# Kernel tuning notes

Measured on AMD Instinct MI355X. Metric: run time of the kernel, lower is better.

## Reference

```python
import jax, jax.numpy as jnp
import numpy as np

B, S, H = 2, 2048, 2048
E, K, HID = 8, 2, 4096          # num_experts, top-k, expert hidden (2*H)
NH, HD = 8, 256                  # attention heads, head_dim
MS, MD = 256, 512                # memory_size, memory_dim
RSTEPS, RD = 3, 512              # reasoning steps, reasoning_dim
SCALE = 16.0                     # sqrt(head_dim)


def setup_inputs() -> dict:
    key = jax.random.key(0)
    ks = iter(jax.random.split(key, 64))
    def w(shape, s=0.02):
        return (jax.random.normal(next(ks), shape, jnp.float32) * s)
    z = lambda *shape: jnp.zeros(shape, jnp.float32)
    inp = {
        'hidden_states': jax.random.normal(next(ks), (B, S, H), jnp.float32),
        'attention_mask': jnp.zeros((B, S), jnp.float32),  # 0 = unmasked (faithful: mask*-1e9 added)
        # MoE
        'gate_w': w((H, E)), 'gate_b': z(E),
        'moe_w1': w((E, H, HID)), 'moe_b1': z(E, HID),
        'moe_w2': w((E, HID, H)), 'moe_b2': z(E, H),
        # memory-augmented attention
        'q_w': w((H, H)), 'q_b': z(H),
        'k_w': w((H, H)), 'k_b': z(H),
        'v_w': w((H, H)), 'v_b': z(H),
        'o_w': w((H, H)), 'o_b': z(H),
        'mem_values': jax.random.normal(next(ks), (MS, MD), jnp.float32),
        'mem_proj_w': w((MD, H)), 'mem_proj_b': z(H),
        'mem_attn_w': w((H, MS)), 'mem_attn_b': z(MS),
        # hierarchical reasoning (stacked over steps)
        'rs_w1': w((RSTEPS, H, RD)), 'rs_b1': z(RSTEPS, RD),
        'rs_w2': w((RSTEPS, RD, H)), 'rs_b2': z(RSTEPS, H),
        'ln_g': jnp.ones((RSTEPS, H), jnp.float32), 'ln_b': z(RSTEPS, H),
        'hg_w1': w((RSTEPS, H, H // 4)), 'hg_b1': z(RSTEPS, H // 4),
        'hg_w2': w((RSTEPS, H // 4, 1)), 'hg_b2': z(RSTEPS, 1),
        'integ_w': w((RSTEPS * H, H)), 'integ_b': z(H),
    }
    return inp


def _layernorm(x, g, b, eps=1e-5):
    m = x.mean(-1, keepdims=True)
    v = ((x - m) ** 2).mean(-1, keepdims=True)
    return (x - m) / jnp.sqrt(v + eps) * g + b


def _forward(hidden_states, attention_mask, gate_w, gate_b, moe_w1, moe_b1, moe_w2, moe_b2,
             q_w, q_b, k_w, k_b, v_w, v_b, o_w, o_b, mem_values, mem_proj_w, mem_proj_b,
             mem_attn_w, mem_attn_b, rs_w1, rs_b1, rs_w2, rs_b2, ln_g, ln_b,
             hg_w1, hg_b1, hg_w2, hg_b2, integ_w, integ_b):
    h = hidden_states
    N = B * S
    # ---- Mixture of Experts (top-k routing, dense combine-weight formulation) ----
    x_flat = h.reshape(N, H)
    gate_probs = jax.nn.softmax(x_flat @ gate_w + gate_b, axis=-1)        # [N,E]
    topk_s, topk_i = jax.lax.top_k(gate_probs, K)                          # [N,K]
    topk_p = jax.nn.softmax(topk_s, axis=-1)                               # renormalize over top-k
    comb = jnp.zeros((N, E), x_flat.dtype).at[jnp.arange(N)[:, None], topk_i].add(topk_p)
    h1 = jax.nn.relu(jnp.einsum('nd,edh->neh', x_flat, moe_w1) + moe_b1)   # [N,E,HID]
    eo = jnp.einsum('neh,ehd->ned', h1, moe_w2) + moe_b2                   # [N,E,H]
    moe_out = jnp.einsum('ned,ne->nd', eo, comb).reshape(B, S, H)
    h = h + 0.5 * moe_out
    # ---- Memory-augmented attention ----
    q = (h @ q_w + q_b).reshape(B, S, NH, HD).transpose(0, 2, 1, 3)
    k = (h @ k_w + k_b).reshape(B, S, NH, HD).transpose(0, 2, 1, 3)
    v = (h @ v_w + v_b).reshape(B, S, NH, HD).transpose(0, 2, 1, 3)
    scores = jnp.einsum('bhqd,bhkd->bhqk', q, k) / SCALE
    scores = scores + attention_mask[:, None, None, :] * (-1e9)
    probs = jax.nn.softmax(scores, axis=-1)
    attn = jnp.einsum('bhqk,bhkd->bhqd', probs, v).transpose(0, 2, 1, 3).reshape(B, S, H)
    mem_p = jax.nn.softmax(h @ mem_attn_w + mem_attn_b, axis=-1)           # [B,S,MS]
    mem_o = (mem_p @ mem_values) @ mem_proj_w + mem_proj_b                 # [B,S,H]
    mem_out = (attn + 0.3 * mem_o) @ o_w + o_b
    h = h + mem_out
    # ---- Hierarchical reasoning ----
    cur = h
    outs = []
    for i in range(RSTEPS):
        so = jax.nn.relu(cur @ rs_w1[i] + rs_b1[i]) @ rs_w2[i] + rs_b2[i]
        so = _layernorm(so, ln_g[i], ln_b[i])
        g = jax.nn.sigmoid(jax.nn.relu(cur @ hg_w1[i] + hg_b1[i]) @ hg_w2[i] + hg_b2[i])  # [B,S,1]
        cur = cur + g * so
        outs.append(cur)
    final = jnp.concatenate(outs, axis=-1) @ integ_w + integ_b
    return h + final


def reference(hidden_states, attention_mask, gate_w, gate_b, moe_w1, moe_b1, moe_w2, moe_b2,
              q_w, q_b, k_w, k_b, v_w, v_b, o_w, o_b, mem_values, mem_proj_w, mem_proj_b,
              mem_attn_w, mem_attn_b, rs_w1, rs_b1, rs_w2, rs_b2, ln_g, ln_b,
              hg_w1, hg_b1, hg_w2, hg_b2, integ_w, integ_b):
    return _forward(hidden_states, attention_mask, gate_w, gate_b, moe_w1, moe_b1, moe_w2, moe_b2,
                    q_w, q_b, k_w, k_b, v_w, v_b, o_w, o_b, mem_values, mem_proj_w, mem_proj_b,
                    mem_attn_w, mem_attn_b, rs_w1, rs_b1, rs_w2, rs_b2, ln_g, ln_b,
                    hg_w1, hg_b1, hg_w2, hg_b2, integ_w, integ_b)
```

## Files before the change

### kernel.cpp

```cpp
#include <hip/hip_runtime.h>
#include <string.h>


typedef __attribute__((ext_vector_type(4))) float f32x4;
typedef __attribute__((ext_vector_type(8))) __bf16 bf16x8;

#define NTOK 4096
#define HDIM 2048

__device__ __forceinline__ unsigned short f2bf(float f) {
  unsigned u = __float_as_uint(f);
  unsigned r = (u + 0x7fffu + ((u >> 16) & 1u)) >> 16;
  return (unsigned short)r;
}
__device__ __forceinline__ float bf2f(unsigned short u) {
  return __uint_as_float(((unsigned)u) << 16);
}
__device__ __forceinline__ void unpack8(uint4 r, float* v) {
  v[0]=bf2f((unsigned short)(r.x&0xffff)); v[1]=bf2f((unsigned short)(r.x>>16));
  v[2]=bf2f((unsigned short)(r.y&0xffff)); v[3]=bf2f((unsigned short)(r.y>>16));
  v[4]=bf2f((unsigned short)(r.z&0xffff)); v[5]=bf2f((unsigned short)(r.z>>16));
  v[6]=bf2f((unsigned short)(r.w&0xffff)); v[7]=bf2f((unsigned short)(r.w>>16));
}
__device__ __forceinline__ uint4 pack8(const float* v) {
  uint4 r;
  r.x = (unsigned)f2bf(v[0]) | ((unsigned)f2bf(v[1])<<16);
  r.y = (unsigned)f2bf(v[2]) | ((unsigned)f2bf(v[3])<<16);
  r.z = (unsigned)f2bf(v[4]) | ((unsigned)f2bf(v[5])<<16);
  r.w = (unsigned)f2bf(v[6]) | ((unsigned)f2bf(v[7])<<16);
  return r;
}

__global__ void k_tconv(const float* __restrict__ in, unsigned short* __restrict__ out,
                        int R, int C, long inB, long outB) {
  __shared__ float tl[32][33];
  const int z = blockIdx.z;
  const float* ip = in + (long)z * inB;
  unsigned short* op = out + (long)z * outB;
  const int tx = threadIdx.x & 31, ty = threadIdx.x >> 5;
  const int c0 = blockIdx.x * 32, r0 = blockIdx.y * 32;
#pragma unroll
  for (int i = 0; i < 4; i++)
    tl[ty + i*8][tx] = ip[(long)(r0 + ty + i*8) * C + c0 + tx];
  __syncthreads();
#pragma unroll
  for (int i = 0; i < 4; i++)
    op[(long)(c0 + ty + i*8) * R + r0 + tx] = f2bf(tl[tx][ty + i*8]);
}

__global__ void k_cvt(const float* __restrict__ in, unsigned short* __restrict__ out, long n4) {
  long i = (long)blockIdx.x * blockDim.x + threadIdx.x;
  if (i < n4) {
    float4 v = ((const float4*)in)[i];
    float vv[4] = {v.x, v.y, v.z, v.w};
    union { unsigned short u[4]; uint2 d; } p;
#pragma unroll
    for (int j = 0; j < 4; j++) p.u[j] = f2bf(vv[j]);
    ((uint2*)out)[i] = p.d;
  }
}

__global__ void k_tvact(const unsigned short* __restrict__ qkv, unsigned short* __restrict__ vT) {
  __shared__ unsigned short tl[32][33];
  const int z = blockIdx.z, b = z >> 3, hh = z & 7;
  const unsigned short* ip = qkv + (long)b * 2048 * 6144 + 4096 + hh * 256;
  unsigned short* op = vT + (long)z * 256 * 2048;
  const int tx = threadIdx.x & 31, ty = threadIdx.x >> 5;
  const int d0 = blockIdx.x * 32, s0 = blockIdx.y * 32;
#pragma unroll
  for (int i = 0; i < 4; i++)
    tl[ty + i*8][tx] = ip[(long)(s0 + ty + i*8) * 6144 + d0 + tx];
  __syncthreads();
#pragma unroll
  for (int i = 0; i < 4; i++)
    op[(long)(d0 + ty + i*8) * 2048 + s0 + tx] = tl[tx][ty + i*8];
}

__global__ void k_maskvec(const float* __restrict__ m, float* __restrict__ mv) {
  int i = blockIdx.x * 256 + threadIdx.x;
  if (i < 4096) mv[i] = -1e9f * m[i];
}

__global__ void k_zero(int* p) { if (threadIdx.x < 8) p[threadIdx.x] = 0; }

__global__ void k_cat3(const float* __restrict__ a, const float* __restrict__ b,
                       const float* __restrict__ c, float* __restrict__ o) {
  int i = blockIdx.x * 256 + threadIdx.x;
  if (i < 2048) { o[i] = a[i]; o[2048 + i] = b[i]; o[4096 + i] = c[i]; }
}

__global__ void k_cat2x3(const float* __restrict__ a, const float* __restrict__ b,
                         float* __restrict__ o) {
  int i = blockIdx.x * 256 + threadIdx.x;
  if (i < 1536) { int s = i >> 9, c = i & 511; o[s * 1024 + c] = a[i]; o[s * 1024 + 512 + c] = b[i]; }
}

__global__ void k_gate(const float* __restrict__ x, const float* __restrict__ gw,
                       const float* __restrict__ gb, int* __restrict__ meta,
                       int* __restrict__ e0a, int* __restrict__ e1a,
                       float* __restrict__ w0a, float* __restrict__ w1a) {
  const int wv = threadIdx.x >> 6, ln = threadIdx.x & 63;
  const int n = blockIdx.x * 4 + wv;
  const float* xr = x + (long)n * HDIM;
  float s[8] = {0,0,0,0,0,0,0,0};
  for (int k = ln; k < HDIM; k += 64) {
    float xv = xr[k];
    const float* g = gw + (long)k * 8;
#pragma unroll
    for (int e = 0; e < 8; e++) s[e] += xv * g[e];
  }
#pragma unroll
  for (int e = 0; e < 8; e++)
    for (int d = 32; d; d >>= 1) s[e] += __shfl_xor(s[e], d);
  if (ln == 0) {
    float mx = -1e30f;
#pragma unroll
    for (int e = 0; e < 8; e++) { s[e] += gb[e]; mx = fmaxf(mx, s[e]); }
    float p[8], sum = 0.f;
#pragma unroll
    for (int e = 0; e < 8; e++) { p[e] = expf(s[e] - mx); sum += p[e]; }
    float inv = 1.f / sum;
#pragma unroll
    for (int e = 0; e < 8; e++) p[e] *= inv;
    int e0 = 0;
    for (int e = 1; e < 8; e++) if (p[e] > p[e0]) e0 = e;
    int e1 = (e0 == 0) ? 1 : 0;
    for (int e = 0; e < 8; e++) if (e != e0 && p[e] > p[e1]) e1 = e;
    float q = expf(p[e1] - p[e0]);
    float w0 = 1.f / (1.f + q), w1 = q / (1.f + q);
    e0a[n] = e0; e1a[n] = e1; w0a[n] = w0; w1a[n] = w1;
    atomicAdd(&meta[e0], 1); atomicAdd(&meta[e1], 1);
  }
}

__global__ void k_buildmap(int* meta) {
  if (threadIdx.x == 0 && blockIdx.x == 0) {
    int cum = 0, nT = 0;
    for (int e = 0; e < 8; e++) {
      int c = meta[e];
      meta[16 + e] = cum; meta[24 + e] = cum + c; meta[8 + e] = 0;
      int t = (c + 127) >> 7;
      for (int i = 0; i < t; i++) { meta[33 + nT] = e; meta[129 + nT] = cum + i * 128; nT++; }
      cum += c;
    }
    meta[32] = nT;
  }
}

__global__ void k_scatter(int* __restrict__ meta, const int* __restrict__ e0a,
                          const int* __restrict__ e1a, int* __restrict__ s0a,
                          int* __restrict__ s1a, int* __restrict__ srcTok) {
  const int n = blockIdx.x * 256 + threadIdx.x;
  if (n < NTOK) {
    int e0 = e0a[n], e1 = e1a[n];
    int s0 = meta[16 + e0] + atomicAdd(&meta[8 + e0], 1);
    int s1 = meta[16 + e1] + atomicAdd(&meta[8 + e1], 1);
    s0a[n] = s0; s1a[n] = s1; srcTok[s0] = n; srcTok[s1] = n;
  }
}

__global__ void k_gather(const unsigned short* __restrict__ xb, const int* __restrict__ srcTok,
                         unsigned short* __restrict__ xg) {
  const int r = blockIdx.x;
  int n = srcTok[r]; if (n < 0 || n >= NTOK) n = 0;
  ((uint4*)(xg + (long)r * HDIM))[threadIdx.x] =
      ((const uint4*)(xb + (long)n * HDIM))[threadIdx.x];
}

__global__ void k_combine(const float* __restrict__ h, const unsigned short* __restrict__ eo,
                          const int* __restrict__ s0a, const int* __restrict__ s1a,
                          const float* __restrict__ w0a, const float* __restrict__ w1a,
                          float* __restrict__ h2, unsigned short* __restrict__ h2b) {
  const int n = blockIdx.x, c = threadIdx.x * 8;
  const float w0 = w0a[n], w1 = w1a[n];
  uint4 a = *(const uint4*)(eo + (long)s0a[n] * HDIM + c);
  uint4 b = *(const uint4*)(eo + (long)s1a[n] * HDIM + c);
  float va[8], vb[8]; unpack8(a, va); unpack8(b, vb);
  const float* hr = h + (long)n * HDIM + c;
  float o[8];
#pragma unroll
  for (int j = 0; j < 8; j++) o[j] = hr[j] + 0.5f * (w0 * va[j] + w1 * vb[j]);
  float* h2r = h2 + (long)n * HDIM + c;
#pragma unroll
  for (int j = 0; j < 8; j++) h2r[j] = o[j];
  *(uint4*)(h2b + (long)n * HDIM + c) = pack8(o);
}

__global__ void k_softmax2048(unsigned short* __restrict__ p) {
  const long r = blockIdx.x;
  unsigned short* row = p + r * 2048;
  const int t = threadIdx.x, wv = t >> 6, ln = t & 63;
  uint4 raw = ((const uint4*)row)[t];
  float v[8]; unpack8(raw, v);
  float m = v[0];
#pragma unroll
  for (int j = 1; j < 8; j++) m = fmaxf(m, v[j]);
  for (int d = 32; d; d >>= 1) m = fmaxf(m, __shfl_xor(m, d));
  __shared__ float sm[4], ssum[4];
  if (ln == 0) sm[wv] = m;
  __syncthreads();
  m = fmaxf(fmaxf(sm[0], sm[1]), fmaxf(sm[2], sm[3]));
  float s = 0.f;
#pragma unroll
  for (int j = 0; j < 8; j++) { v[j] = expf(v[j] - m); s += v[j]; }
  for (int d = 32; d; d >>= 1) s += __shfl_xor(s, d);
  if (ln == 0) ssum[wv] = s;
  __syncthreads();
  s = ssum[0] + ssum[1] + ssum[2] + ssum[3];
  const float inv = 1.f / s;
#pragma unroll
  for (int j = 0; j < 8; j++) v[j] *= inv;
  ((uint4*)row)[t] = pack8(v);
}

__global__ void k_softmax256(const float* __restrict__ in, unsigned short* __restrict__ out) {
  const int wv = threadIdx.x >> 6, ln = threadIdx.x & 63;
  const long r = (long)blockIdx.x * 4 + wv;
  const float4 v4 = ((const float4*)(in + r * 256))[ln];
  float v[4] = {v4.x, v4.y, v4.z, v4.w};
  float m = fmaxf(fmaxf(v[0], v[1]), fmaxf(v[2], v[3]));
  for (int d = 32; d; d >>= 1) m = fmaxf(m, __shfl_xor(m, d));
  float s = 0.f;
#pragma unroll
  for (int j = 0; j < 4; j++) { v[j] = expf(v[j] - m); s += v[j]; }
  for (int d = 32; d; d >>= 1) s += __shfl_xor(s, d);
  const float inv = 1.f / s;
  union { unsigned short u[4]; uint2 d2; } p;
#pragma unroll
  for (int j = 0; j < 4; j++) p.u[j] = f2bf(v[j] * inv);
  ((uint2*)(out + r * 256))[ln] = p.d2;
}

__global__ void k_gdot(const unsigned short* __restrict__ g1, long ld, const float* __restrict__ w,
                       const float* __restrict__ bb, float* __restrict__ gv) {
  const int wv = threadIdx.x >> 6, ln = threadIdx.x & 63;
  const int n = blockIdx.x * 4 + wv;
  uint4 raw = *(const uint4*)(g1 + (long)n * ld + ln * 8);
  float v[8]; unpack8(raw, v);
  const float4 wa = ((const float4*)w)[ln * 2];
  const float4 wb = ((const float4*)w)[ln * 2 + 1];
  float s = v[0]*wa.x + v[1]*wa.y + v[2]*wa.z + v[3]*wa.w
          + v[4]*wb.x + v[5]*wb.y + v[6]*wb.z + v[7]*wb.w;
  for (int d = 32; d; d >>= 1) s += __shfl_xor(s, d);
  if (ln == 0) gv[n] = 1.f / (1.f + expf(-(s + bb[0])));
}

__global__ void k_lnupdate(const float* __restrict__ so, const float* __restrict__ curIn,
                           const float* __restrict__ gv, const float* __restrict__ lng,
                           const float* __restrict__ lnb, float* __restrict__ curOut,
                           unsigned short* __restrict__ curbOut, unsigned short* __restrict__ outs,
                           int step) {
  const int n = blockIdx.x, t = threadIdx.x, wv = t >> 6, ln = t & 63, c = t * 8;
  const float* row = so + (long)n * 2048 + c;
  float x[8];
#pragma unroll
  for (int j = 0; j < 8; j++) x[j] = row[j];
  float s1 = 0.f, s2 = 0.f;
#pragma unroll
  for (int j = 0; j < 8; j++) { s1 += x[j]; s2 += x[j] * x[j]; }
  for (int d = 32; d; d >>= 1) { s1 += __shfl_xor(s1, d); s2 += __shfl_xor(s2, d); }
  __shared__ float a1[4], a2[4];
  if (ln == 0) { a1[wv] = s1; a2[wv] = s2; }
  __syncthreads();
  s1 = a1[0] + a1[1] + a1[2] + a1[3];
  s2 = a2[0] + a2[1] + a2[2] + a2[3];
  const float mean = s1 * (1.f / 2048.f);
  const float var = s2 * (1.f / 2048.f) - mean * mean;
  const float rstd = rsqrtf(var + 1e-5f);
  const float g = gv[n];
  const float* ci = curIn + (long)n * 2048 + c;
  float o[8];
#pragma unroll
  for (int j = 0; j < 8; j++) {
    float l = (x[j] - mean) * rstd * lng[c + j] + lnb[c + j];
    o[j] = ci[j] + g * l;
  }
  float* co = curOut + (long)n * 2048 + c;
#pragma unroll
  for (int j = 0; j < 8; j++) co[j] = o[j];
  *(uint4*)(curbOut + (long)n * 2048 + c) = pack8(o);
  *(uint4*)(outs + (long)n * 6144 + (long)step * 2048 + c) = pack8(o);
}

struct GArgs {
  const unsigned short* A; long lda, aSO, aSI;
  const unsigned short* Bt; long ldb, bSO, bSI;
  int M, N, K;
  const float* adv; long advSO, advSI;
  float alpha, rscale;
  const float* rF; long ldrF, rfSO, rfSI;
  const unsigned short* rB; long ldrB, rbSO, rbSI;
  float* oF; long ldoF, ofSO, ofSI;
  unsigned short* oB; long ldoB, obSO, obSI;
  const int* meta;
};

#define LDS_A_ELEM 8192
#define LDS_BUF_ELEM 24576
template <int MOE, int RELU, int RESID, int OUTF, int OUTB>
__global__ __launch_bounds__(512) void gemm_bt(GArgs g) {
  __shared__ unsigned short lds[3 * LDS_BUF_ELEM];
  const int t = threadIdx.x, wv = t >> 6, ln = t & 63;
  const int lr8 = ln >> 3;
  const int lsl = (ln & 7) ^ lr8;
  const int bz = blockIdx.z;
  int row0, rowMax;
  const unsigned short *A, *Bt;
  long advO = 0, rFO = 0, rBO = 0, oFO = 0, oBO = 0;
  if constexpr (MOE) {
    const int ty = blockIdx.y;
    if (ty >= g.meta[32]) return;
    const int e = g.meta[33 + ty];
    row0 = g.meta[129 + ty]; rowMax = g.meta[24 + e];
    A = g.A; Bt = g.Bt + (long)e * g.bSO;
    advO = (long)e * g.advSO;
  } else {
    row0 = blockIdx.y << 7; rowMax = g.M;
    const long bo = (long)(bz >> 3), bi = (long)(bz & 7);
    A = g.A + bo * g.aSO + bi * g.aSI;
    Bt = g.Bt + bo * g.bSO + bi * g.bSI;
    advO = bo * g.advSO + bi * g.advSI;
    rFO = bo * g.rfSO + bi * g.rfSI;
    rBO = bo * g.rbSO + bi * g.rbSI;
    oFO = bo * g.ofSO + bi * g.ofSI;
    oBO = bo * g.obSO + bi * g.obSI;
  }
  const int col0 = blockIdx.x << 8;
  const long lda = g.lda, ldb = g.ldb;

  auto STAGE = [&](int kt, unsigned bufOff) {
    const long kk = ((long)kt << 6) + (lsl << 3);
#pragma unroll
    for (int l = 0; l < 2; ++l) {
      const int r = (l << 6) + (wv << 3) + lr8;
      int gr = row0 + r;
      if constexpr (MOE) gr = (gr < rowMax) ? gr : (rowMax - 1);
      __builtin_amdgcn_global_load_lds(
          (const __attribute__((address_space(1))) void*)(A + (long)gr * lda + kk),
          (__attribute__((address_space(3))) void*)(lds + bufOff + ((l << 9) + (wv << 6)) * 8),
          16, 0, 0);
    }
#pragma unroll
    for (int l = 0; l < 4; ++l) {
      const int r = (l << 6) + (wv << 3) + lr8;
      __builtin_amdgcn_global_load_lds(
          (const __attribute__((address_space(1))) void*)(Bt + (long)(col0 + r) * ldb + kk),
          (__attribute__((address_space(3))) void*)(lds + bufOff + LDS_A_ELEM + ((l << 9) + (wv << 6)) * 8),
          16, 0, 0);
    }
  };

  const f32x4 fz = {0.f, 0.f, 0.f, 0.f};
  f32x4 acc[4][4];
#pragma unroll
  for (int i = 0; i < 4; i++)
#pragma unroll
    for (int j = 0; j < 4; j++) acc[i][j] = fz;

  const int wr = (wv >> 2) << 6;
  const int wc = (wv & 3) << 6;
  const int nt = g.K >> 6;

  unsigned cur = 0, nxt = LDS_BUF_ELEM, nx2 = 2 * LDS_BUF_ELEM;
  STAGE(0, cur); STAGE(1, nxt);
  for (int kt = 0; kt < nt; ++kt) {
    if (kt + 2 < nt) {
      STAGE(kt + 2, nx2);
      asm volatile("s_waitcnt vmcnt(12)" ::: "memory");
    } else if (kt + 1 < nt) {
      asm volatile("s_waitcnt vmcnt(6)" ::: "memory");
    } else {
      asm volatile("s_waitcnt vmcnt(0)" ::: "memory");
    }
    __builtin_amdgcn_s_barrier();
    {
      const unsigned aB = cur, bB = cur + LDS_A_ELEM;
#pragma unroll
      for (int ks = 0; ks < 2; ++ks) {
        bf16x8 af[4], bg[4];
        const int kb = (ks << 2) + (ln >> 4);
#pragma unroll
        for (int i = 0; i < 4; ++i) {
          const int r = wr + (i << 4) + (ln & 15);
          af[i] = *(const bf16x8*)(lds + aB + (r << 6) + ((kb ^ (r & 7)) << 3));
        }
#pragma unroll
        for (int j = 0; j < 4; ++j) {
          const int r = wc + (j << 4) + (ln & 15);
          bg[j] = *(const bf16x8*)(lds + bB + (r << 6) + ((kb ^ (r & 7)) << 3));
        }
        __builtin_amdgcn_s_setprio(1);
#pragma unroll
        for (int i = 0; i < 4; ++i)
#pragma unroll
          for (int j = 0; j < 4; ++j)
            acc[i][j] = __builtin_amdgcn_mfma_f32_16x16x32_bf16(af[i], bg[j], acc[i][j], 0, 0, 0);
        __builtin_amdgcn_s_setprio(0);
      }
    }
    __builtin_amdgcn_s_barrier();
    const unsigned tmp = cur; cur = nxt; nxt = nx2; nx2 = tmp;
  }

#pragma unroll
  for (int i = 0; i < 4; i++) {
#pragma unroll
    for (int j = 0; j < 4; j++) {
      const int cc = col0 + wc + (j << 4) + (ln & 15);
      const float av = g.adv ? g.adv[advO + cc] : 0.f;
#pragma unroll
      for (int r = 0; r < 4; r++) {
        const int rr = row0 + wr + (i << 4) + ((ln >> 4) << 2) + r;
        if (rr < rowMax) {
          float v = g.alpha * acc[i][j][r] + av;
          if constexpr (RELU) v = fmaxf(v, 0.f);
          if constexpr (RESID == 1) v = g.rF[rFO + (long)rr * g.ldrF + cc] + g.rscale * v;
          if constexpr (RESID == 2) v = bf2f(g.rB[rBO + (long)rr * g.ldrB + cc]) + g.rscale * v;
          if constexpr (OUTF) g.oF[oFO + (long)rr * g.ldoF + cc] = v;
          if constexpr (OUTB) g.oB[oBO + (long)rr * g.ldoB + cc] = f2bf(v);
        }
      }
    }
  }
}

static constexpr size_t O_W1T = 0;
static constexpr size_t O_W2T = O_W1T + (size_t)8 * 4096 * 2048 * 2;
static constexpr size_t O_QT  = O_W2T + (size_t)8 * 4096 * 2048 * 2;
static constexpr size_t O_KT  = O_QT + (size_t)2048 * 2048 * 2;
static constexpr size_t O_VWT = O_KT + (size_t)2048 * 2048 * 2;
static constexpr size_t O_OT  = O_VWT + (size_t)2048 * 2048 * 2;
static constexpr size_t O_MAT = O_OT + (size_t)2048 * 2048 * 2;
static constexpr size_t O_MPT = O_MAT + (size_t)256 * 2048 * 2;
static constexpr size_t O_MVT = O_MPT + (size_t)2048 * 512 * 2;
static constexpr size_t O_RH1 = O_MVT + (size_t)512 * 256 * 2;
static constexpr size_t O_RS2 = O_RH1 + (size_t)3 * 1024 * 2048 * 2;
static constexpr size_t O_IGT = O_RS2 + (size_t)3 * 2048 * 512 * 2;
static constexpr size_t O_META= O_IGT + (size_t)2048 * 6144 * 2;
static constexpr size_t O_E0  = O_META + 4096;
static constexpr size_t O_E1  = O_E0 + 16384;
static constexpr size_t O_W0  = O_E1 + 16384;
static constexpr size_t O_W1  = O_W0 + 16384;
static constexpr size_t O_S0  = O_W1 + 16384;
static constexpr size_t O_S1  = O_S0 + 16384;
static constexpr size_t O_SRC = O_S1 + 16384;
static constexpr size_t O_MSK = O_SRC + 32768;
static constexpr size_t O_GV  = O_MSK + 16384;
static constexpr size_t O_QKVB= O_GV + 16384;
static constexpr size_t O_RHB = O_QKVB + 6144 * 4;
static constexpr size_t O_H2  = O_RHB + 3072 * 4;
static constexpr size_t O_H2B = O_H2 + (size_t)4096 * 2048 * 4;
static constexpr size_t O_H3  = O_H2B + (size_t)4096 * 2048 * 2;
static constexpr size_t O_H3B = O_H3 + (size_t)4096 * 2048 * 4;
static constexpr size_t O_ATT = O_H3B + (size_t)4096 * 2048 * 2;
static constexpr size_t O_AO2 = O_ATT + (size_t)4096 * 2048 * 2;
static constexpr size_t O_MLG = O_AO2 + (size_t)4096 * 2048 * 2;
static constexpr size_t O_MPB = O_MLG + (size_t)4096 * 256 * 4;
static constexpr size_t O_MPV = O_MPB + (size_t)4096 * 256 * 2;
static constexpr size_t O_AR  = O_MPV + (size_t)4096 * 512 * 2;
static constexpr size_t O_XB = O_AR;
static constexpr size_t O_XG = O_XB + (size_t)4096 * 2048 * 2;
static constexpr size_t O_H1 = O_XG + (size_t)8192 * 2048 * 2;
static constexpr size_t O_EO = O_H1 + (size_t)8192 * 4096 * 2;
static constexpr size_t O_QB = O_AR;
static constexpr size_t O_VT = O_QB + (size_t)3 * 4096 * 2048 * 2;
static constexpr size_t O_SC = O_VT + (size_t)4096 * 2048 * 2;
static constexpr size_t O_T1 = O_AR;
static constexpr size_t O_SOB= O_T1 + (size_t)4096 * 1024 * 2;
static constexpr size_t O_CUR= O_SOB + (size_t)4096 * 2048 * 4;
static constexpr size_t O_CRB= O_CUR + (size_t)4096 * 2048 * 4;
static constexpr size_t O_OUS= O_CRB + (size_t)4096 * 2048 * 2;

extern "C" void kernel_launch(void* const* d_in, const int* in_sizes, int n_in,
                              void* d_out, int out_size, void* d_ws, size_t ws_size,
                              hipStream_t stream) {
  (void)in_sizes; (void)n_in; (void)out_size; (void)ws_size;
  const float* h        = (const float*)d_in[0];
  const float* mask     = (const float*)d_in[1];
  const float* gate_w   = (const float*)d_in[2];
  const float* gate_b   = (const float*)d_in[3];
  const float* moe_w1   = (const float*)d_in[4];
  const float* moe_b1   = (const float*)d_in[5];
  const float* moe_w2   = (const float*)d_in[6];
  const float* moe_b2   = (const float*)d_in[7];
  const float* q_w      = (const float*)d_in[8];
  const float* q_b      = (const float*)d_in[9];
  const float* k_w      = (const float*)d_in[10];
  const float* k_b      = (const float*)d_in[11];
  const float* v_w      = (const float*)d_in[12];
  const float* v_b      = (const float*)d_in[13];
  const float* o_w      = (const float*)d_in[14];
  const float* o_b      = (const float*)d_in[15];
  const float* mem_vals = (const float*)d_in[16];
  const float* mproj_w  = (const float*)d_in[17];
  const float* mproj_b  = (const float*)d_in[18];
  const float* mattn_w  = (const float*)d_in[19];
  const float* mattn_b  = (const float*)d_in[20];
  const float* rs_w1    = (const float*)d_in[21];
  const float* rs_b1    = (const float*)d_in[22];
  const float* rs_w2    = (const float*)d_in[23];
  const float* rs_b2    = (const float*)d_in[24];
  const float* ln_g     = (const float*)d_in[25];
  const float* ln_b     = (const float*)d_in[26];
  const float* hg_w1    = (const float*)d_in[27];
  const float* hg_b1    = (const float*)d_in[28];
  const float* hg_w2    = (const float*)d_in[29];
  const float* hg_b2    = (const float*)d_in[30];
  const float* integ_w  = (const float*)d_in[31];
  const float* integ_b  = (const float*)d_in[32];

  char* ws = (char*)d_ws;
  auto U = [&](size_t o) { return (unsigned short*)(ws + o); };
  auto F = [&](size_t o) { return (float*)(ws + o); };
  auto I = [&](size_t o) { return (int*)(ws + o); };

  k_tconv<<<dim3(128, 64, 8), 256, 0, stream>>>(moe_w1, U(O_W1T), 2048, 4096, 8388608, 8388608);
  k_tconv<<<dim3(64, 128, 8), 256, 0, stream>>>(moe_w2, U(O_W2T), 4096, 2048, 8388608, 8388608);
  k_tconv<<<dim3(64, 64, 1), 256, 0, stream>>>(q_w, U(O_QT), 2048, 2048, 0, 0);
  k_tconv<<<dim3(64, 64, 1), 256, 0, stream>>>(k_w, U(O_KT), 2048, 2048, 0, 0);
  k_tconv<<<dim3(64, 64, 1), 256, 0, stream>>>(v_w, U(O_VWT), 2048, 2048, 0, 0);
  k_tconv<<<dim3(64, 64, 1), 256, 0, stream>>>(o_w, U(O_OT), 2048, 2048, 0, 0);
  k_tconv<<<dim3(8, 64, 1), 256, 0, stream>>>(mattn_w, U(O_MAT), 2048, 256, 0, 0);
  k_tconv<<<dim3(64, 16, 1), 256, 0, stream>>>(mproj_w, U(O_MPT), 512, 2048, 0, 0);
  k_tconv<<<dim3(16, 8, 1), 256, 0, stream>>>(mem_vals, U(O_MVT), 256, 512, 0, 0);
  k_tconv<<<dim3(16, 64, 3), 256, 0, stream>>>(rs_w1, U(O_RH1), 2048, 512, 2048 * 512, 1024 * 2048);
  k_tconv<<<dim3(16, 64, 3), 256, 0, stream>>>(hg_w1, U(O_RH1) + (size_t)512 * 2048, 2048, 512,
                                               2048 * 512, 1024 * 2048);
  k_tconv<<<dim3(64, 16, 3), 256, 0, stream>>>(rs_w2, U(O_RS2), 512, 2048, 512 * 2048, 512 * 2048);
  k_tconv<<<dim3(64, 192, 1), 256, 0, stream>>>(integ_w, U(O_IGT), 6144, 2048, 0, 0);
  k_cvt<<<8192, 256, 0, stream>>>(h, U(O_XB), 2097152);
  k_maskvec<<<16, 256, 0, stream>>>(mask, F(O_MSK));
  k_cat3<<<8, 256, 0, stream>>>(q_b, k_b, v_b, F(O_QKVB));
  k_cat2x3<<<6, 256, 0, stream>>>(rs_b1, hg_b1, F(O_RHB));
  k_zero<<<1, 64, 0, stream>>>(I(O_META));

  k_gate<<<1024, 256, 0, stream>>>(h, gate_w, gate_b, I(O_META), I(O_E0), I(O_E1), F(O_W0), F(O_W1));
  k_buildmap<<<1, 1, 0, stream>>>(I(O_META));
  k_scatter<<<16, 256, 0, stream>>>(I(O_META), I(O_E0), I(O_E1), I(O_S0), I(O_S1), I(O_SRC));
  k_gather<<<8192, 256, 0, stream>>>(U(O_XB), I(O_SRC), U(O_XG));

  GArgs z0; memset(&z0, 0, sizeof(z0)); z0.alpha = 1.f; z0.rscale = 1.f;
  {
    GArgs g = z0;
    g.A = U(O_XG); g.lda = 2048;
    g.Bt = U(O_W1T); g.ldb = 2048; g.bSO = (long)4096 * 2048;
    g.N = 4096; g.K = 2048;
    g.adv = moe_b1; g.advSO = 4096;
    g.oB = U(O_H1); g.ldoB = 4096;
    g.meta = I(O_META);
    gemm_bt<1, 1, 0, 0, 1><<<dim3(16, 72, 1), 512, 0, stream>>>(g);
  }
  {
    GArgs g = z0;
    g.A = U(O_H1); g.lda = 4096;
    g.Bt = U(O_W2T); g.ldb = 4096; g.bSO = (long)2048 * 4096;
    g.N = 2048; g.K = 4096;
    g.adv = moe_b2; g.advSO = 2048;
    g.oB = U(O_EO); g.ldoB = 2048;
    g.meta = I(O_META);
    gemm_bt<1, 0, 0, 0, 1><<<dim3(8, 72, 1), 512, 0, stream>>>(g);
  }
  k_combine<<<4096, 256, 0, stream>>>(h, U(O_EO), I(O_S0), I(O_S1), F(O_W0), F(O_W1),
                                      F(O_H2), U(O_H2B));

  {
    GArgs g = z0;
    g.A = U(O_H2B); g.lda = 2048; g.M = 4096; g.N = 6144; g.K = 2048;
    g.Bt = U(O_QT); g.ldb = 2048;
    g.adv = F(O_QKVB);
    g.oB = U(O_QB); g.ldoB = 6144;
    gemm_bt<0, 0, 0, 0, 1><<<dim3(24, 32, 1), 512, 0, stream>>>(g);
  }
  k_tvact<<<dim3(8, 64, 16), 256, 0, stream>>>(U(O_QB), U(O_VT));
  {
    GArgs g = z0;
    g.A = U(O_QB); g.lda = 6144; g.aSO = 12582912; g.aSI = 256;
    g.Bt = U(O_QB) + 2048; g.ldb = 6144; g.bSO = 12582912; g.bSI = 256;
    g.M = 2048; g.N = 2048; g.K = 256;
    g.adv = F(O_MSK); g.advSO = 2048; g.advSI = 0;
    g.alpha = 0.0625f;
    g.oB = U(O_SC); g.ldoB = 2048; g.obSO = 33554432; g.obSI = 4194304;
    gemm_bt<0, 0, 0, 0, 1><<<dim3(8, 16, 16), 512, 0, stream>>>(g);
  }
  k_softmax2048<<<32768, 256, 0, stream>>>(U(O_SC));
  {
    GArgs g = z0;
    g.A = U(O_SC); g.lda = 2048; g.aSO = 33554432; g.aSI = 4194304;
    g.Bt = U(O_VT); g.ldb = 2048; g.bSO = 4194304; g.bSI = 524288;
    g.M = 2048; g.N = 256; g.K = 2048;
    g.oB = U(O_ATT); g.ldoB = 2048; g.obSO = 4194304; g.obSI = 256;
    gemm_bt<0, 0, 0, 0, 1><<<dim3(1, 16, 16), 512, 0, stream>>>(g);
  }
  {
    GArgs g = z0;
    g.A = U(O_H2B); g.lda = 2048; g.Bt = U(O_MAT); g.ldb = 2048;
    g.M = 4096; g.N = 256; g.K = 2048;
    g.adv = mattn_b;
    g.oF = F(O_MLG); g.ldoF = 256;
    gemm_bt<0, 0, 0, 1, 0><<<dim3(1, 32, 1), 512, 0, stream>>>(g);
  }
  k_softmax256<<<1024, 256, 0, stream>>>(F(O_MLG), U(O_MPB));
  {
    GArgs g = z0;
    g.A = U(O_MPB); g.lda = 256; g.Bt = U(O_MVT); g.ldb = 256;
    g.M = 4096; g.N = 512; g.K = 256;
    g.oB = U(O_MPV); g.ldoB = 512;
    gemm_bt<0, 0, 0, 0, 1><<<dim3(2, 32, 1), 512, 0, stream>>>(g);
  }
  {
    GArgs g = z0;
    g.A = U(O_MPV); g.lda = 512; g.Bt = U(O_MPT); g.ldb = 512;
    g.M = 4096; g.N = 2048; g.K = 512;
    g.adv = mproj_b;
    g.rB = U(O_ATT); g.ldrB = 2048; g.rscale = 0.3f;
    g.oB = U(O_AO2); g.ldoB = 2048;
    gemm_bt<0, 0, 2, 0, 1><<<dim3(8, 32, 1), 512, 0, stream>>>(g);
  }
  {
    GArgs g = z0;
    g.A = U(O_AO2); g.lda = 2048; g.Bt = U(O_OT); g.ldb = 2048;
    g.M = 4096; g.N = 2048; g.K = 2048;
    g.adv = o_b;
    g.rF = F(O_H2); g.ldrF = 2048; g.rscale = 1.f;
    g.oF = F(O_H3); g.ldoF = 2048;
    g.oB = U(O_H3B); g.ldoB = 2048;
    gemm_bt<0, 0, 1, 1, 1><<<dim3(8, 32, 1), 512, 0, stream>>>(g);
  }

  for (int i = 0; i < 3; i++) {
    const unsigned short* curb = (i == 0) ? U(O_H3B) : U(O_CRB);
    const float* curf = (i == 0) ? F(O_H3) : F(O_CUR);
    {
      GArgs g = z0;
      g.A = curb; g.lda = 2048;
      g.Bt = U(O_RH1) + (size_t)i * 1024 * 2048; g.ldb = 2048;
      g.M = 4096; g.N = 1024; g.K = 2048;
      g.adv = F(O_RHB) + i * 1024;
      g.oB = U(O_T1); g.ldoB = 1024;
      gemm_bt<0, 1, 0, 0, 1><<<dim3(4, 32, 1), 512, 0, stream>>>(g);
    }
    {
      GArgs g = z0;
      g.A = U(O_T1); g.lda = 1024;
      g.Bt = U(O_RS2) + (size_t)i * 2048 * 512; g.ldb = 512;
      g.M = 4096; g.N = 2048; g.K = 512;
      g.adv = rs_b2 + i * 2048;
      g.oF = F(O_SOB); g.ldoF = 2048;
      gemm_bt<0, 0, 0, 1, 0><<<dim3(8, 32, 1), 512, 0, stream>>>(g);
    }
    k_gdot<<<1024, 256, 0, stream>>>(U(O_T1) + 512, 1024, hg_w2 + i * 512, hg_b2 + i, F(O_GV));
    k_lnupdate<<<4096, 256, 0, stream>>>(F(O_SOB), curf, F(O_GV), ln_g + i * 2048,
                                         ln_b + i * 2048, F(O_CUR), U(O_CRB), U(O_OUS), i);
  }
  {
    GArgs g = z0;
    g.A = U(O_OUS); g.lda = 6144; g.Bt = U(O_IGT); g.ldb = 6144;
    g.M = 4096; g.N = 2048; g.K = 6144;
    g.adv = integ_b;
    g.rF = F(O_H3); g.ldrF = 2048; g.rscale = 1.f;
    g.oF = (float*)d_out; g.ldoF = 2048;
    gemm_bt<0, 0, 1, 1, 0><<<dim3(8, 32, 1), 512, 0, stream>>>(g);
  }
}
```

Baseline: 1.946 ms.

## Shrink GEMM tile to 128x128 with double-buffered LDS and prefetch after fragment loads

The shared bf16 GEMM now uses 128x128 output tiles (from 128x256), with each wave computing 64x32. The LDS scheme drops from a triple buffer to a double buffer, and the next k-tile is issued only after the current fragments have been read into registers. Every launch doubles its grid in x to match. This cuts LDS use and accumulator registers, which should raise occupancy and block count. In exchange it lowers arithmetic intensity per block, and the full vmcnt(0) wait each iteration exposes more load latency.

```diff
diff --git a/kernel.cpp b/kernel.cpp
--- a/kernel.cpp
+++ b/kernel.cpp
@@ -7,6 +7,8 @@
 
 #define NTOK 4096
 #define HDIM 2048
+#define AS1 __attribute__((address_space(1)))
+#define AS3 __attribute__((address_space(3)))
 
 __device__ __forceinline__ unsigned short f2bf(float f) {
   unsigned u = __float_as_uint(f);
@@ -295,12 +297,10 @@
   const int* meta;
 };
 
-#define LDS_A_ELEM 8192
-#define LDS_BUF_ELEM 24576
 template <int MOE, int RELU, int RESID, int OUTF, int OUTB>
 __global__ __launch_bounds__(512) void gemm_bt(GArgs g) {
-  __shared__ unsigned short lds[3 * LDS_BUF_ELEM];
-  const int t = threadIdx.x, wv = t >> 6, ln = t & 63;
+  __shared__ unsigned short lds[2 * 16384];
+  const int t = threadIdx.x, wv = t >> 6, ln = t & 63, ln15 = ln & 15;
   const int lr8 = ln >> 3;
   const int lsl = (ln & 7) ^ lr8;
   const int bz = blockIdx.z;
@@ -325,92 +325,87 @@
     oFO = bo * g.ofSO + bi * g.ofSI;
     oBO = bo * g.obSO + bi * g.obSI;
   }
-  const int col0 = blockIdx.x << 8;
+  const int col0 = blockIdx.x << 7;
   const long lda = g.lda, ldb = g.ldb;
-
-  auto STAGE = [&](int kt, unsigned bufOff) {
+  const int wm = (wv >> 2) << 6;
+  const int wc = (wv & 3) << 5;
+
+  auto STAGE = [&](int kt, unsigned base) {
     const long kk = ((long)kt << 6) + (lsl << 3);
 #pragma unroll
     for (int l = 0; l < 2; ++l) {
-      const int r = (l << 6) + (wv << 3) + lr8;
-      int gr = row0 + r;
+      const int rb = (wv << 4) + (l << 3);
+      int gr = row0 + rb + lr8;
       if constexpr (MOE) gr = (gr < rowMax) ? gr : (rowMax - 1);
       __builtin_amdgcn_global_load_lds(
-          (const __attribute__((address_space(1))) void*)(A + (long)gr * lda + kk),
-          (__attribute__((address_space(3))) void*)(lds + bufOff + ((l << 9) + (wv << 6)) * 8),
-          16, 0, 0);
+          (const AS1 void*)(A + (long)gr * lda + kk),
+          (AS3 void*)(lds + base + (rb << 6)), 16, 0, 0);
     }
 #pragma unroll
-    for (int l = 0; l < 4; ++l) {
-      const int r = (l << 6) + (wv << 3) + lr8;
+    for (int l = 0; l < 2; ++l) {
+      const int rb = (wv << 4) + (l << 3);
       __builtin_amdgcn_global_load_lds(
-          (const __attribute__((address_space(1))) void*)(Bt + (long)(col0 + r) * ldb + kk),
-          (__attribute__((address_space(3))) void*)(lds + bufOff + LDS_A_ELEM + ((l << 9) + (wv << 6)) * 8),
-          16, 0, 0);
+          (const AS1 void*)(Bt + (long)(col0 + rb + lr8) * ldb + kk),
+          (AS3 void*)(lds + base + 8192 + (rb << 6)), 16, 0, 0);
     }
   };
 
   const f32x4 fz = {0.f, 0.f, 0.f, 0.f};
-  f32x4 acc[4][4];
+  f32x4 acc[4][2];
 #pragma unroll
   for (int i = 0; i < 4; i++)
 #pragma unroll
-    for (int j = 0; j < 4; j++) acc[i][j] = fz;
-
-  const int wr = (wv >> 2) << 6;
-  const int wc = (wv & 3) << 6;
+    for (int j = 0; j < 2; j++) acc[i][j] = fz;
+
   const int nt = g.K >> 6;
 
-  unsigned cur = 0, nxt = LDS_BUF_ELEM, nx2 = 2 * LDS_BUF_ELEM;
-  STAGE(0, cur); STAGE(1, nxt);
+  STAGE(0, 0);
+  asm volatile("s_waitcnt vmcnt(0)" ::: "memory");
+  __builtin_amdgcn_s_barrier();
+
   for (int kt = 0; kt < nt; ++kt) {
-    if (kt + 2 < nt) {
-      STAGE(kt + 2, nx2);
-      asm volatile("s_waitcnt vmcnt(12)" ::: "memory");
-    } else if (kt + 1 < nt) {
-      asm volatile("s_waitcnt vmcnt(6)" ::: "memory");
-    } else {
-      asm volatile("s_waitcnt vmcnt(0)" ::: "memory");
-    }
-    __builtin_amdgcn_s_barrier();
-    {
-      const unsigned aB = cur, bB = cur + LDS_A_ELEM;
-#pragma unroll
-      for (int ks = 0; ks < 2; ++ks) {
-        bf16x8 af[4], bg[4];
-        const int kb = (ks << 2) + (ln >> 4);
-#pragma unroll
-        for (int i = 0; i < 4; ++i) {
-          const int r = wr + (i << 4) + (ln & 15);
-          af[i] = *(const bf16x8*)(lds + aB + (r << 6) + ((kb ^ (r & 7)) << 3));
-        }
-#pragma unroll
-        for (int j = 0; j < 4; ++j) {
-          const int r = wc + (j << 4) + (ln & 15);
-          bg[j] = *(const bf16x8*)(lds + bB + (r << 6) + ((kb ^ (r & 7)) << 3));
-        }
-        __builtin_amdgcn_s_setprio(1);
-#pragma unroll
-        for (int i = 0; i < 4; ++i)
-#pragma unroll
-          for (int j = 0; j < 4; ++j)
-            acc[i][j] = __builtin_amdgcn_mfma_f32_16x16x32_bf16(af[i], bg[j], acc[i][j], 0, 0, 0);
-        __builtin_amdgcn_s_setprio(0);
+    const unsigned aB = (kt & 1) ? 16384u : 0u;
+    const unsigned nB = aB ^ 16384u;
+    bf16x8 af[2][4], bg[2][2];
+#pragma unroll
+    for (int ks = 0; ks < 2; ++ks) {
+      const int kb = (ks << 2) + (ln >> 4);
+#pragma unroll
+      for (int i = 0; i < 4; ++i) {
+        const int r = wm + (i << 4) + ln15;
+        af[ks][i] = *(const bf16x8*)(lds + aB + (r << 6) + ((kb ^ (r & 7)) << 3));
+      }
+#pragma unroll
+      for (int j = 0; j < 2; ++j) {
+        const int r = wc + (j << 4) + ln15;
+        bg[ks][j] = *(const bf16x8*)(lds + aB + 8192 + (r << 6) + ((kb ^ (r & 7)) << 3));
       }
     }
+    __builtin_amdgcn_sched_barrier(0);
+    if (kt + 1 < nt) STAGE(kt + 1, nB);
+    __builtin_amdgcn_sched_barrier(0);
+    __builtin_amdgcn_s_setprio(1);
+#pragma unroll
+    for (int ks = 0; ks < 2; ++ks)
+#pragma unroll
+      for (int i = 0; i < 4; ++i)
+#pragma unroll
+        for (int j = 0; j < 2; ++j)
+          acc[i][j] = __builtin_amdgcn_mfma_f32_16x16x32_bf16(af[ks][i], bg[ks][j], acc[i][j], 0, 0, 0);
+    __builtin_amdgcn_s_setprio(0);
+    asm volatile("s_waitcnt vmcnt(0)" ::: "memory");
     __builtin_amdgcn_s_barrier();
-    const unsigned tmp = cur; cur = nxt; nxt = nx2; nx2 = tmp;
   }
 
 #pragma unroll
   for (int i = 0; i < 4; i++) {
 #pragma unroll
-    for (int j = 0; j < 4; j++) {
-      const int cc = col0 + wc + (j << 4) + (ln & 15);
+    for (int j = 0; j < 2; j++) {
+      const int cc = col0 + wc + (j << 4) + ln15;
       const float av = g.adv ? g.adv[advO + cc] : 0.f;
 #pragma unroll
       for (int r = 0; r < 4; r++) {
-        const int rr = row0 + wr + (i << 4) + ((ln >> 4) << 2) + r;
+        const int rr = row0 + wm + (i << 4) + ((ln >> 4) << 2) + r;
         if (rr < rowMax) {
           float v = g.alpha * acc[i][j][r] + av;
           if constexpr (RELU) v = fmaxf(v, 0.f);
@@ -548,7 +543,7 @@
     g.adv = moe_b1; g.advSO = 4096;
     g.oB = U(O_H1); g.ldoB = 4096;
     g.meta = I(O_META);
-    gemm_bt<1, 1, 0, 0, 1><<<dim3(16, 72, 1), 512, 0, stream>>>(g);
+    gemm_bt<1, 1, 0, 0, 1><<<dim3(32, 72, 1), 512, 0, stream>>>(g);
   }
   {
     GArgs g = z0;
@@ -558,7 +553,7 @@
     g.adv = moe_b2; g.advSO = 2048;
     g.oB = U(O_EO); g.ldoB = 2048;
     g.meta = I(O_META);
-    gemm_bt<1, 0, 0, 0, 1><<<dim3(8, 72, 1), 512, 0, stream>>>(g);
+    gemm_bt<1, 0, 0, 0, 1><<<dim3(16, 72, 1), 512, 0, stream>>>(g);
   }
   k_combine<<<4096, 256, 0, stream>>>(h, U(O_EO), I(O_S0), I(O_S1), F(O_W0), F(O_W1),
                                       F(O_H2), U(O_H2B));
@@ -569,7 +564,7 @@
     g.Bt = U(O_QT); g.ldb = 2048;
     g.adv = F(O_QKVB);
     g.oB = U(O_QB); g.ldoB = 6144;
-    gemm_bt<0, 0, 0, 0, 1><<<dim3(24, 32, 1), 512, 0, stream>>>(g);
+    gemm_bt<0, 0, 0, 0, 1><<<dim3(48, 32, 1), 512, 0, stream>>>(g);
   }
   k_tvact<<<dim3(8, 64, 16), 256, 0, stream>>>(U(O_QB), U(O_VT));
   {
@@ -580,7 +575,7 @@
     g.adv = F(O_MSK); g.advSO = 2048; g.advSI = 0;
     g.alpha = 0.0625f;
     g.oB = U(O_SC); g.ldoB = 2048; g.obSO = 33554432; g.obSI = 4194304;
-    gemm_bt<0, 0, 0, 0, 1><<<dim3(8, 16, 16), 512, 0, stream>>>(g);
+    gemm_bt<0, 0, 0, 0, 1><<<dim3(16, 16, 16), 512, 0, stream>>>(g);
   }
   k_softmax2048<<<32768, 256, 0, stream>>>(U(O_SC));
   {
@@ -589,7 +584,7 @@
     g.Bt = U(O_VT); g.ldb = 2048; g.bSO = 4194304; g.bSI = 524288;
     g.M = 2048; g.N = 256; g.K = 2048;
     g.oB = U(O_ATT); g.ldoB = 2048; g.obSO = 4194304; g.obSI = 256;
-    gemm_bt<0, 0, 0, 0, 1><<<dim3(1, 16, 16), 512, 0, stream>>>(g);
+    gemm_bt<0, 0, 0, 0, 1><<<dim3(2, 16, 16), 512, 0, stream>>>(g);
   }
   {
     GArgs g = z0;
@@ -597,7 +592,7 @@
     g.M = 4096; g.N = 256; g.K = 2048;
     g.adv = mattn_b;
     g.oF = F(O_MLG); g.ldoF = 256;
-    gemm_bt<0, 0, 0, 1, 0><<<dim3(1, 32, 1), 512, 0, stream>>>(g);
+    gemm_bt<0, 0, 0, 1, 0><<<dim3(2, 32, 1), 512, 0, stream>>>(g);
   }
   k_softmax256<<<1024, 256, 0, stream>>>(F(O_MLG), U(O_MPB));
   {
@@ -605,7 +600,7 @@
     g.A = U(O_MPB); g.lda = 256; g.Bt = U(O_MVT); g.ldb = 256;
     g.M = 4096; g.N = 512; g.K = 256;
     g.oB = U(O_MPV); g.ldoB = 512;
-    gemm_bt<0, 0, 0, 0, 1><<<dim3(2, 32, 1), 512, 0, stream>>>(g);
+    gemm_bt<0, 0, 0, 0, 1><<<dim3(4, 32, 1), 512, 0, stream>>>(g);
   }
   {
     GArgs g = z0;
@@ -614,7 +609,7 @@
     g.adv = mproj_b;
     g.rB = U(O_ATT); g.ldrB = 2048; g.rscale = 0.3f;
     g.oB = U(O_AO2); g.ldoB = 2048;
-    gemm_bt<0, 0, 2, 0, 1><<<dim3(8, 32, 1), 512, 0, stream>>>(g);
+    gemm_bt<0, 0, 2, 0, 1><<<dim3(16, 32, 1), 512, 0, stream>>>(g);
   }
   {
     GArgs g = z0;
@@ -624,7 +619,7 @@
     g.rF = F(O_H2); g.ldrF = 2048; g.rscale = 1.f;
     g.oF = F(O_H3); g.ldoF = 2048;
     g.oB = U(O_H3B); g.ldoB = 2048;
-    gemm_bt<0, 0, 1, 1, 1><<<dim3(8, 32, 1), 512, 0, stream>>>(g);
+    gemm_bt<0, 0, 1, 1, 1><<<dim3(16, 32, 1), 512, 0, stream>>>(g);
   }
 
   for (int i = 0; i < 3; i++) {
@@ -637,7 +632,7 @@
       g.M = 4096; g.N = 1024; g.K = 2048;
       g.adv = F(O_RHB) + i * 1024;
       g.oB = U(O_T1); g.ldoB = 1024;
-      gemm_bt<0, 1, 0, 0, 1><<<dim3(4, 32, 1), 512, 0, stream>>>(g);
+      gemm_bt<0, 1, 0, 0, 1><<<dim3(8, 32, 1), 512, 0, stream>>>(g);
     }
     {
       GArgs g = z0;
@@ -646,7 +641,7 @@
       g.M = 4096; g.N = 2048; g.K = 512;
       g.adv = rs_b2 + i * 2048;
       g.oF = F(O_SOB); g.ldoF = 2048;
-      gemm_bt<0, 0, 0, 1, 0><<<dim3(8, 32, 1), 512, 0, stream>>>(g);
+      gemm_bt<0, 0, 0, 1, 0><<<dim3(16, 32, 1), 512, 0, stream>>>(g);
     }
     k_gdot<<<1024, 256, 0, stream>>>(U(O_T1) + 512, 1024, hg_w2 + i * 512, hg_b2 + i, F(O_GV));
     k_lnupdate<<<4096, 256, 0, stream>>>(F(O_SOB), curf, F(O_GV), ln_g + i * 2048,
@@ -659,6 +654,6 @@
     g.adv = integ_b;
     g.rF = F(O_H3); g.ldrF = 2048; g.rscale = 1.f;
     g.oF = (float*)d_out; g.ldoF = 2048;
-    gemm_bt<0, 0, 1, 1, 0><<<dim3(8, 32, 1), 512, 0, stream>>>(g);
-  }
-}
+    gemm_bt<0, 0, 1, 1, 0><<<dim3(16, 32, 1), 512, 0, stream>>>(g);
+  }
+}
```

Measured after the change: 1.738 ms. -10.7%, faster.

## Replace triple-buffered GEMM pipeline with single-buffer high-occupancy kernel and XCD-aware block remap

Applied to the files above, without the earlier changes.

Drops the three-stage LDS ring (144KB) for a single 48KB buffer with __syncthreads, and adds launch_bounds(512,4) so more blocks can be resident per CU, relying on occupancy rather than software pipelining to hide load latency. It also remaps block indices so that consecutive logical tiles land on the same XCD, which should improve L2 reuse. A-fragment loads now happen inside the MFMA loop to cut register pressure. The risk is exposed global-load latency, since each k-tile now waits on its own loads and takes two barriers.

```diff
diff --git a/kernel.cpp b/kernel.cpp
--- a/kernel.cpp
+++ b/kernel.cpp
@@ -7,6 +7,8 @@
 
 #define NTOK 4096
 #define HDIM 2048
+#define AS1 __attribute__((address_space(1)))
+#define AS3 __attribute__((address_space(3)))
 
 __device__ __forceinline__ unsigned short f2bf(float f) {
   unsigned u = __float_as_uint(f);
@@ -295,27 +297,35 @@
   const int* meta;
 };
 
-#define LDS_A_ELEM 8192
-#define LDS_BUF_ELEM 24576
 template <int MOE, int RELU, int RESID, int OUTF, int OUTB>
-__global__ __launch_bounds__(512) void gemm_bt(GArgs g) {
-  __shared__ unsigned short lds[3 * LDS_BUF_ELEM];
-  const int t = threadIdx.x, wv = t >> 6, ln = t & 63;
+__global__ __launch_bounds__(512, 4) void gemm_bt(GArgs g) {
+  __shared__ unsigned short lds[24576];
+  const int t = threadIdx.x, wv = t >> 6, ln = t & 63, ln15 = ln & 15;
   const int lr8 = ln >> 3;
   const int lsl = (ln & 7) ^ lr8;
   const int bz = blockIdx.z;
+
+  int bx, by;
+  {
+    const int gx = gridDim.x, gyd = gridDim.y;
+    const int n = gx * gyd;
+    const int s = blockIdx.y * gx + blockIdx.x;
+    const int q = n >> 3, r = n & 7, xcd = s & 7, i = s >> 3;
+    const int lg = (xcd < r) ? (xcd * (q + 1) + i) : (r * (q + 1) + (xcd - r) * q + i);
+    bx = lg / gyd; by = lg - bx * gyd;
+  }
+
   int row0, rowMax;
   const unsigned short *A, *Bt;
   long advO = 0, rFO = 0, rBO = 0, oFO = 0, oBO = 0;
   if constexpr (MOE) {
-    const int ty = blockIdx.y;
-    if (ty >= g.meta[32]) return;
-    const int e = g.meta[33 + ty];
-    row0 = g.meta[129 + ty]; rowMax = g.meta[24 + e];
+    if (by >= g.meta[32]) return;
+    const int e = g.meta[33 + by];
+    row0 = g.meta[129 + by]; rowMax = g.meta[24 + e];
     A = g.A; Bt = g.Bt + (long)e * g.bSO;
     advO = (long)e * g.advSO;
   } else {
-    row0 = blockIdx.y << 7; rowMax = g.M;
+    row0 = by << 7; rowMax = g.M;
     const long bo = (long)(bz >> 3), bi = (long)(bz & 7);
     A = g.A + bo * g.aSO + bi * g.aSI;
     Bt = g.Bt + bo * g.bSO + bi * g.bSI;
@@ -325,92 +335,71 @@
     oFO = bo * g.ofSO + bi * g.ofSI;
     oBO = bo * g.obSO + bi * g.obSI;
   }
-  const int col0 = blockIdx.x << 8;
+  const int col0 = bx << 8;
   const long lda = g.lda, ldb = g.ldb;
-
-  auto STAGE = [&](int kt, unsigned bufOff) {
+  const int wm = (wv >> 2) << 6;
+  const int wn = (wv & 3) << 6;
+
+  const f32x4 fz = {0.f, 0.f, 0.f, 0.f};
+  f32x4 acc[4][4];
+#pragma unroll
+  for (int i = 0; i < 4; i++)
+#pragma unroll
+    for (int j = 0; j < 4; j++) acc[i][j] = fz;
+
+  const int nt = g.K >> 6;
+
+  for (int kt = 0; kt < nt; ++kt) {
     const long kk = ((long)kt << 6) + (lsl << 3);
 #pragma unroll
     for (int l = 0; l < 2; ++l) {
-      const int r = (l << 6) + (wv << 3) + lr8;
-      int gr = row0 + r;
+      const int rb = (wv << 4) + (l << 3);
+      int gr = row0 + rb + lr8;
       if constexpr (MOE) gr = (gr < rowMax) ? gr : (rowMax - 1);
       __builtin_amdgcn_global_load_lds(
-          (const __attribute__((address_space(1))) void*)(A + (long)gr * lda + kk),
-          (__attribute__((address_space(3))) void*)(lds + bufOff + ((l << 9) + (wv << 6)) * 8),
-          16, 0, 0);
+          (const AS1 void*)(A + (long)gr * lda + kk),
+          (AS3 void*)(lds + (rb << 6)), 16, 0, 0);
     }
 #pragma unroll
     for (int l = 0; l < 4; ++l) {
-      const int r = (l << 6) + (wv << 3) + lr8;
+      const int rb = (l << 6) + (wv << 3);
       __builtin_amdgcn_global_load_lds(
-          (const __attribute__((address_space(1))) void*)(Bt + (long)(col0 + r) * ldb + kk),
-          (__attribute__((address_space(3))) void*)(lds + bufOff + LDS_A_ELEM + ((l << 9) + (wv << 6)) * 8),
-          16, 0, 0);
+          (const AS1 void*)(Bt + (long)(col0 + rb + lr8) * ldb + kk),
+          (AS3 void*)(lds + 8192 + (rb << 6)), 16, 0, 0);
     }
-  };
-
-  const f32x4 fz = {0.f, 0.f, 0.f, 0.f};
-  f32x4 acc[4][4];
-#pragma unroll
-  for (int i = 0; i < 4; i++)
-#pragma unroll
-    for (int j = 0; j < 4; j++) acc[i][j] = fz;
-
-  const int wr = (wv >> 2) << 6;
-  const int wc = (wv & 3) << 6;
-  const int nt = g.K >> 6;
-
-  unsigned cur = 0, nxt = LDS_BUF_ELEM, nx2 = 2 * LDS_BUF_ELEM;
-  STAGE(0, cur); STAGE(1, nxt);
-  for (int kt = 0; kt < nt; ++kt) {
-    if (kt + 2 < nt) {
-      STAGE(kt + 2, nx2);
-      asm volatile("s_waitcnt vmcnt(12)" ::: "memory");
-    } else if (kt + 1 < nt) {
-      asm volatile("s_waitcnt vmcnt(6)" ::: "memory");
-    } else {
-      asm volatile("s_waitcnt vmcnt(0)" ::: "memory");
+    __syncthreads();
+#pragma unroll
+    for (int ks = 0; ks < 2; ++ks) {
+      const int kb = (ks << 2) + (ln >> 4);
+      bf16x8 bg[4];
+#pragma unroll
+      for (int j = 0; j < 4; ++j) {
+        const int r = wn + (j << 4) + ln15;
+        bg[j] = *(const bf16x8*)(lds + 8192 + (r << 6) + ((kb ^ (r & 7)) << 3));
+      }
+      __builtin_amdgcn_s_setprio(1);
+#pragma unroll
+      for (int i = 0; i < 4; ++i) {
+        const int r = wm + (i << 4) + ln15;
+        bf16x8 a = *(const bf16x8*)(lds + (r << 6) + ((kb ^ (r & 7)) << 3));
+#pragma unroll
+        for (int j = 0; j < 4; ++j)
+          acc[i][j] = __builtin_amdgcn_mfma_f32_16x16x32_bf16(a, bg[j], acc[i][j], 0, 0, 0);
+      }
+      __builtin_amdgcn_s_setprio(0);
     }
-    __builtin_amdgcn_s_barrier();
-    {
-      const unsigned aB = cur, bB = cur + LDS_A_ELEM;
-#pragma unroll
-      for (int ks = 0; ks < 2; ++ks) {
-        bf16x8 af[4], bg[4];
-        const int kb = (ks << 2) + (ln >> 4);
-#pragma unroll
-        for (int i = 0; i < 4; ++i) {
-          const int r = wr + (i << 4) + (ln & 15);
-          af[i] = *(const bf16x8*)(lds + aB + (r << 6) + ((kb ^ (r & 7)) << 3));
-        }
-#pragma unroll
-        for (int j = 0; j < 4; ++j) {
-          const int r = wc + (j << 4) + (ln & 15);
-          bg[j] = *(const bf16x8*)(lds + bB + (r << 6) + ((kb ^ (r & 7)) << 3));
-        }
-        __builtin_amdgcn_s_setprio(1);
-#pragma unroll
-        for (int i = 0; i < 4; ++i)
-#pragma unroll
-          for (int j = 0; j < 4; ++j)
-            acc[i][j] = __builtin_amdgcn_mfma_f32_16x16x32_bf16(af[i], bg[j], acc[i][j], 0, 0, 0);
-        __builtin_amdgcn_s_setprio(0);
-      }
-    }
-    __builtin_amdgcn_s_barrier();
-    const unsigned tmp = cur; cur = nxt; nxt = nx2; nx2 = tmp;
+    __syncthreads();
   }
 
 #pragma unroll
   for (int i = 0; i < 4; i++) {
 #pragma unroll
     for (int j = 0; j < 4; j++) {
-      const int cc = col0 + wc + (j << 4) + (ln & 15);
+      const int cc = col0 + wn + (j << 4) + ln15;
       const float av = g.adv ? g.adv[advO + cc] : 0.f;
 #pragma unroll
       for (int r = 0; r < 4; r++) {
-        const int rr = row0 + wr + (i << 4) + ((ln >> 4) << 2) + r;
+        const int rr = row0 + wm + (i << 4) + ((ln >> 4) << 2) + r;
         if (rr < rowMax) {
           float v = g.alpha * acc[i][j][r] + av;
           if constexpr (RELU) v = fmaxf(v, 0.f);
```

Measured after the change: 2.113 ms. +8.6%, slower.
